# Kernel tuning notes

Measured on AMD Instinct MI355X. Metric: run time of the kernel, lower is better.

The kernel has to match this reference:

```python
import jax, jax.numpy as jnp
import numpy as np
from jax import lax

D_MODEL = 64
D_STATE = 16
D_CONV = 3
EXPAND = 2
D_INNER = EXPAND * D_MODEL  # 128
DT_RANK = (D_MODEL + 15) // 16  # 4
B, H, W = 2, 64, 64


def setup_inputs() -> dict:
    key = jax.random.key(0)
    ks = jax.random.split(key, 8)
    def n(k, shape, s=0.02):
        return jax.random.normal(k, shape, dtype=jnp.float32) * s
    return {
        "x": jax.random.normal(ks[0], (B, D_MODEL, H, W), dtype=jnp.float32),
        "ln_w": jnp.ones((D_MODEL,), jnp.float32),
        "ln_b": jnp.zeros((D_MODEL,), jnp.float32),
        "W_in": n(ks[1], (4, 2 * D_INNER, D_MODEL)),          # in_proj per direction
        "conv_w": n(ks[2], (4, D_INNER, 1, D_CONV), 0.1),     # depthwise causal conv
        "conv_b": jnp.zeros((4, D_INNER), jnp.float32),
        "W_xproj": n(ks[3], (4, DT_RANK + 2 * D_STATE, D_INNER)),
        "W_dt": n(ks[4], (4, D_INNER, DT_RANK), 0.1),
        "b_dt": n(ks[5], (4, D_INNER), 0.1),
        "A_log": jnp.log(jnp.broadcast_to(jnp.arange(1, D_STATE + 1, dtype=jnp.float32), (4, D_INNER, D_STATE))),
        "D_param": jnp.ones((4, D_INNER), jnp.float32),
        "W_out": n(ks[6], (4, D_MODEL, D_INNER)),
    }


def _mamba(x, W_in, conv_w, conv_b, W_xproj, W_dt, b_dt, A_log, Dp, W_out):
    # x: (B, L, D) -> (B, L, D). Standard Mamba forward with selective scan.
    xz = x @ W_in.T                              # (B, L, 2*d_inner)
    xp, z = jnp.split(xz, 2, axis=-1)
    xc = jnp.swapaxes(xp, 1, 2)                  # (B, d_inner, L)
    xc = lax.conv_general_dilated(xc, conv_w, (1,), [(D_CONV - 1, 0)], feature_group_count=D_INNER)
    xc = xc + conv_b[None, :, None]
    xp = jax.nn.silu(jnp.swapaxes(xc, 1, 2))     # (B, L, d_inner)
    dbl = xp @ W_xproj.T                         # (B, L, dt_rank + 2*d_state)
    dt = dbl[..., :DT_RANK]
    Bc = dbl[..., DT_RANK:DT_RANK + D_STATE]
    Cc = dbl[..., DT_RANK + D_STATE:]
    dt = jax.nn.softplus(dt @ W_dt.T + b_dt)     # (B, L, d_inner)
    A = -jnp.exp(A_log)                          # (d_inner, d_state)
    dA = jnp.exp(dt[..., None] * A)              # (B, L, d_inner, d_state)
    dBu = (dt * xp)[..., None] * Bc[:, :, None, :]

    def comb(c1, c2):
        a1, b1 = c1
        a2, b2 = c2
        return a1 * a2, a2 * b1 + b2

    _, h = lax.associative_scan(comb, (dA, dBu), axis=1)  # parallel linear recurrence
    y = jnp.einsum('blds,bls->bld', h, Cc) + xp * Dp
    y = y * jax.nn.silu(z)
    return y @ W_out.T


def reference(x, ln_w, ln_b, W_in, conv_w, conv_b, W_xproj, W_dt, b_dt, A_log, D_param, W_out):
    Bq, C, Hh, Ww = x.shape
    xn = jnp.transpose(x, (0, 2, 3, 1))          # (B, H, W, C)
    mu = xn.mean(-1, keepdims=True)
    var = xn.var(-1, keepdims=True)
    xn = (xn - mu) * lax.rsqrt(var + 1e-5) * ln_w + ln_b
    x_f = xn.reshape(Bq, Hh * Ww, C)                              # row-major scan
    x_tf = jnp.transpose(xn, (0, 2, 1, 3)).reshape(Bq, Ww * Hh, C)  # column-major scan
    xs = jnp.stack([x_f, x_f[:, ::-1], x_tf, x_tf[:, ::-1]])      # (4, B, L, C)
    ys = jax.vmap(_mamba)(xs, W_in, conv_w, conv_b, W_xproj, W_dt, b_dt, A_log, D_param, W_out)
    y = ys[0].reshape(Bq, Hh, Ww, C) + ys[1][:, ::-1].reshape(Bq, Hh, Ww, C)
    yt = ys[2].reshape(Bq, Ww, Hh, C) + ys[3][:, ::-1].reshape(Bq, Ww, Hh, C)
    y = y + jnp.transpose(yt, (0, 2, 1, 3))
    return jnp.transpose(y, (0, 3, 1, 2))        # back to (B, C, H, W)
```

## Files before the change

### kernel.cpp

```cpp
#include <hip/hip_runtime.h>
#include <math.h>


#define PP  8
#define LL  4096
#define DD  128
#define SS  16
#define CH  32
#define NCH 128

__device__ __forceinline__ float sigmoidf_(float x){ return 1.0f/(1.0f+__expf(-x)); }

__global__ __launch_bounds__(256) void k_ln(const float* __restrict__ x,
    const float* __restrict__ lw, const float* __restrict__ lb, float* __restrict__ xn) {
  int tid = threadIdx.x;
  int lane = tid & 63;
  int pos = blockIdx.x*4 + (tid>>6);
  int b = pos >> 12, hw = pos & 4095;
  float v = x[((long)(b*64 + lane))*4096 + hw];
  float s = v;
  for (int m = 32; m; m >>= 1) s += __shfl_xor(s, m);
  float mu = s * (1.0f/64.0f);
  float dv = (v-mu)*(v-mu);
  for (int m = 32; m; m >>= 1) dv += __shfl_xor(dv, m);
  float rs = rsqrtf(dv*(1.0f/64.0f) + 1e-5f);
  xn[(long)pos*64 + lane] = (v-mu)*rs*lw[lane] + lb[lane];
}

__global__ __launch_bounds__(256) void k_xseq(const float* __restrict__ xn, float* __restrict__ xseq) {
  int gid = blockIdx.x*256 + threadIdx.x;
  int c = gid & 63;
  int t = (gid >> 6) & 4095;
  int p = gid >> 18;
  int b = p & 1, dir = p >> 1;
  int l;
  if (dir == 0) l = t;
  else if (dir == 1) l = 4095 - t;
  else {
    int tt = (dir == 2) ? t : 4095 - t;
    l = ((tt & 63) << 6) | (tt >> 6);
  }
  xseq[gid] = xn[((long)(b*4096 + l))*64 + c];
}

__global__ __launch_bounds__(256) void k_gemm(const float* __restrict__ A, const float* __restrict__ Bw,
    float* __restrict__ C, int M, int N, int K, long aStr, long bStr, long cStr) {
  __shared__ float Ast[64][68];
  __shared__ float Bst[64][68];
  int pair = blockIdx.z;
  const float* Ap = A + (long)pair*aStr;
  const float* Bp = Bw + (long)(pair>>1)*bStr;
  float* Cp = C + (long)pair*cStr;
  int tid = threadIdx.x;
  int tx = tid & 15, ty = tid >> 4;
  int m0 = blockIdx.x*64, n0 = blockIdx.y*64;
  int kk4 = tid & 15, rr = tid >> 4;
  float acc[4][4] = {};
  for (int ko = 0; ko < K; ko += 64) {
    for (int pass = 0; pass < 4; ++pass) {
      int r = pass*16 + rr;
      float4 av = *(const float4*)(Ap + (long)(m0+r)*K + ko + kk4*4);
      Ast[kk4*4+0][r]=av.x; Ast[kk4*4+1][r]=av.y; Ast[kk4*4+2][r]=av.z; Ast[kk4*4+3][r]=av.w;
      int j = n0 + r;
      float4 bv = make_float4(0.f,0.f,0.f,0.f);
      if (j < N) bv = *(const float4*)(Bp + (long)j*K + ko + kk4*4);
      Bst[kk4*4+0][r]=bv.x; Bst[kk4*4+1][r]=bv.y; Bst[kk4*4+2][r]=bv.z; Bst[kk4*4+3][r]=bv.w;
    }
    __syncthreads();
    #pragma unroll 8
    for (int kk = 0; kk < 64; ++kk) {
      float4 a = *(const float4*)(&Ast[kk][ty*4]);
      float4 b = *(const float4*)(&Bst[kk][tx*4]);
      acc[0][0] += a.x*b.x; acc[0][1] += a.x*b.y; acc[0][2] += a.x*b.z; acc[0][3] += a.x*b.w;
      acc[1][0] += a.y*b.x; acc[1][1] += a.y*b.y; acc[1][2] += a.y*b.z; acc[1][3] += a.y*b.w;
      acc[2][0] += a.z*b.x; acc[2][1] += a.z*b.y; acc[2][2] += a.z*b.z; acc[2][3] += a.z*b.w;
      acc[3][0] += a.w*b.x; acc[3][1] += a.w*b.y; acc[3][2] += a.w*b.z; acc[3][3] += a.w*b.w;
    }
    __syncthreads();
  }
  for (int i = 0; i < 4; ++i)
    for (int j = 0; j < 4; ++j) {
      int m = m0 + ty*4 + i, n = n0 + tx*4 + j;
      if (n < N) Cp[(long)m*N + n] = acc[i][j];
    }
}

__global__ __launch_bounds__(256) void k_conv(const float* __restrict__ xz, const float* __restrict__ cw,
    const float* __restrict__ cb, float* __restrict__ u) {
  int gid = blockIdx.x*256 + threadIdx.x;
  int d = gid & 127;
  int t = (gid >> 7) & 4095;
  int p = gid >> 19;
  int dir = p >> 1;
  const float* base = xz + ((long)p*4096)*256 + d;
  float x2 = base[(long)t*256];
  float x1 = (t >= 1) ? base[(long)(t-1)*256] : 0.f;
  float x0 = (t >= 2) ? base[(long)(t-2)*256] : 0.f;
  const float* w = cw + (dir*128 + d)*3;
  float a = x0*w[0] + x1*w[1] + x2*w[2] + cb[dir*128 + d];
  u[gid] = a * sigmoidf_(a);
}

__global__ __launch_bounds__(256) void k_dt(const float* __restrict__ dbl, const float* __restrict__ wdt,
    const float* __restrict__ bdt, float* __restrict__ dt) {
  int gid = blockIdx.x*256 + threadIdx.x;
  int d = gid & 127;
  int t = (gid >> 7) & 4095;
  int p = gid >> 19;
  int dir = p >> 1;
  const float* r = dbl + ((long)p*4096 + t)*36;
  float4 w = *(const float4*)(wdt + ((dir*128 + d) << 2));
  float lin = r[0]*w.x + r[1]*w.y + r[2]*w.z + r[3]*w.w + bdt[dir*128 + d];
  float sp = (lin > 20.f) ? lin : log1pf(__expf(lin));
  dt[gid] = sp;
}

__global__ __launch_bounds__(128) void k_scan1(const float* __restrict__ dt, const float* __restrict__ u,
    const float* __restrict__ dbl, const float* __restrict__ alog,
    float* __restrict__ pend, float* __restrict__ dAc) {
  int ch = blockIdx.x, p = blockIdx.y, dir = p >> 1;
  int d = threadIdx.x;
  __shared__ float Bsm[CH*16];
  long rowbase = (long)p*LL + ch*CH;
  #pragma unroll
  for (int k = 0; k < 4; ++k) {
    int idx = d + k*128;
    int t = idx >> 4, j = idx & 15;
    Bsm[idx] = dbl[(rowbase + t)*36 + 4 + j];
  }
  float A[16], ps[16];
  const float* ab = alog + ((dir*DD + d) << 4);
  #pragma unroll
  for (int s = 0; s < 16; ++s) { A[s] = -__expf(ab[s]); ps[s] = 0.f; }
  float sd = 0.f;
  __syncthreads();
  for (int t = 0; t < CH; ++t) {
    long row = rowbase + t;
    float dtv = dt[row*DD + d];
    float uv  = u [row*DD + d];
    float dtu = dtv*uv;
    sd += dtv;
    const float* Bs = &Bsm[t*16];
    #pragma unroll
    for (int s = 0; s < 16; ++s) {
      float dA = __expf(dtv*A[s]);
      ps[s] = fmaf(dA, ps[s], dtu*Bs[s]);
    }
  }
  long base = ((long)(p*NCH + ch)*DD + d)*16;
  #pragma unroll
  for (int s = 0; s < 16; ++s) {
    pend[base+s] = ps[s];
    dAc [base+s] = __expf(A[s]*sd);
  }
}

__global__ __launch_bounds__(256) void k_scan2(const float* __restrict__ pend,
    const float* __restrict__ dAc, float* __restrict__ carry) {
  int g = blockIdx.x*256 + threadIdx.x;
  long hi = ((long)(g >> 11)) << 18;
  int lo = g & 2047;
  float c = 0.f;
  for (int chk = 0; chk < NCH; ++chk) {
    long idx = hi + ((long)chk << 11) + lo;
    carry[idx] = c;
    c = fmaf(dAc[idx], c, pend[idx]);
  }
}

__global__ __launch_bounds__(128) void k_scan3(const float* __restrict__ dt, const float* __restrict__ u,
    const float* __restrict__ dbl, const float* __restrict__ xz, const float* __restrict__ alog,
    const float* __restrict__ Dp, const float* __restrict__ carry, float* __restrict__ y) {
  int ch = blockIdx.x, p = blockIdx.y, dir = p >> 1;
  int d = threadIdx.x;
  __shared__ float Bsm[CH*16];
  __shared__ float Csm[CH*16];
  long rowbase = (long)p*LL + ch*CH;
  #pragma unroll
  for (int k = 0; k < 8; ++k) {
    int idx = d + k*128;
    int half = idx >> 9;
    int e = idx & 511;
    int t = e >> 4, j = e & 15;
    float v = dbl[(rowbase + t)*36 + (half ? 20 : 4) + j];
    if (half) Csm[e] = v; else Bsm[e] = v;
  }
  float A[16], h[16];
  const float* ab = alog + ((dir*DD + d) << 4);
  long cbase = ((long)(p*NCH + ch)*DD + d)*16;
  #pragma unroll
  for (int s = 0; s < 16; ++s) {
    A[s] = -__expf(ab[s]);
    h[s] = carry[cbase + s];
  }
  float Dv = Dp[dir*DD + d];
  __syncthreads();
  for (int t = 0; t < CH; ++t) {
    long row = rowbase + t;
    float dtv = dt[row*DD + d];
    float uv  = u [row*DD + d];
    float zv  = xz[row*256 + 128 + d];
    float dtu = dtv*uv;
    const float* Bs = &Bsm[t*16];
    const float* Cs = &Csm[t*16];
    float acc = 0.f;
    #pragma unroll
    for (int s = 0; s < 16; ++s) {
      float dA = __expf(dtv*A[s]);
      h[s] = fmaf(dA, h[s], dtu*Bs[s]);
      acc = fmaf(h[s], Cs[s], acc);
    }
    float yv = acc + uv*Dv;
    yv *= zv * sigmoidf_(zv);
    y[row*DD + d] = yv;
  }
}

__global__ __launch_bounds__(256) void k_comb(const float* __restrict__ yg, float* __restrict__ out) {
  int o = blockIdx.x*256 + threadIdx.x;
  int w = o & 63, h = (o>>6)&63, c = (o>>12)&63, b = o>>18;
  int t0 = (h<<6)|w, t2 = (w<<6)|h;
  float v = yg[((long)(b*4096) + t0)*64 + c]
          + yg[((long)((2+b)*4096) + (4095 - t0))*64 + c]
          + yg[((long)((4+b)*4096) + t2)*64 + c]
          + yg[((long)((6+b)*4096) + (4095 - t2))*64 + c];
  out[o] = v;
}

extern "C" void kernel_launch(void* const* d_in, const int* in_sizes, int n_in,
                              void* d_out, int out_size, void* d_ws, size_t ws_size,
                              hipStream_t stream) {
  const float* x      = (const float*)d_in[0];
  const float* ln_w   = (const float*)d_in[1];
  const float* ln_b   = (const float*)d_in[2];
  const float* W_in   = (const float*)d_in[3];
  const float* conv_w = (const float*)d_in[4];
  const float* conv_b = (const float*)d_in[5];
  const float* W_xp   = (const float*)d_in[6];
  const float* W_dt   = (const float*)d_in[7];
  const float* b_dt   = (const float*)d_in[8];
  const float* A_log  = (const float*)d_in[9];
  const float* D_par  = (const float*)d_in[10];
  const float* W_out  = (const float*)d_in[11];

  float* ws    = (float*)d_ws;
  float* xn    = ws;
  float* xseq  = xn    + 524288;
  float* xz    = xseq  + 2097152;
  float* u     = xz    + 8388608;
  float* dblb  = u     + 4194304;
  float* dtb   = dblb  + 1179648;
  float* ybuf  = dtb   + 4194304;
  float* yg    = ybuf  + 4194304;
  float* pend  = ybuf;
  float* dAc   = ybuf  + 2097152;
  float* carry = xseq;

  k_ln  <<<2048, 256, 0, stream>>>(x, ln_w, ln_b, xn);
  k_xseq<<<8192, 256, 0, stream>>>(xn, xseq);
  k_gemm<<<dim3(64,4,8), 256, 0, stream>>>(xseq, W_in, xz, 4096, 256, 64,
                                           4096L*64, 256L*64, 4096L*256);
  k_conv<<<16384, 256, 0, stream>>>(xz, conv_w, conv_b, u);
  k_gemm<<<dim3(64,1,8), 256, 0, stream>>>(u, W_xp, dblb, 4096, 36, 128,
                                           4096L*128, 36L*128, 4096L*36);
  k_dt  <<<16384, 256, 0, stream>>>(dblb, W_dt, b_dt, dtb);
  k_scan1<<<dim3(NCH,PP), 128, 0, stream>>>(dtb, u, dblb, A_log, pend, dAc);
  k_scan2<<<64, 256, 0, stream>>>(pend, dAc, carry);
  k_scan3<<<dim3(NCH,PP), 128, 0, stream>>>(dtb, u, dblb, xz, A_log, D_par, carry, ybuf);
  k_gemm<<<dim3(64,1,8), 256, 0, stream>>>(ybuf, W_out, yg, 4096, 64, 128,
                                           4096L*128, 64L*128, 4096L*64);
  k_comb<<<2048, 256, 0, stream>>>(yg, (float*)d_out);
}
```

Before: 245.9 us.

## Fuse direction gather into in_proj GEMM and dt projection into scan kernels

Removes the k_xseq permutation kernel by having a specialized in_proj GEMM gather rows from the normalized input through a direction map. Removes the k_dt kernel and its 4M-float buffer by recomputing softplus(dt projection) inside both scan passes from the dbl rows. Reshapes scan2 into more, smaller blocks for more parallelism, and rewrites the final combine to transpose through shared memory so output stores are coalesced. The cost is duplicated dt math in scan1 and scan3 and a separate workspace for carry/pend.

```diff
diff --git a/kernel.cpp b/kernel.cpp
--- a/kernel.cpp
+++ b/kernel.cpp
@@ -5,11 +5,17 @@
 #define PP  8
 #define LL  4096
 #define DD  128
-#define SS  16
 #define CH  32
 #define NCH 128
 
 __device__ __forceinline__ float sigmoidf_(float x){ return 1.0f/(1.0f+__expf(-x)); }
+
+__device__ __forceinline__ int dirmap(int dir, int t) {
+  if (dir == 0) return t;
+  if (dir == 1) return 4095 - t;
+  int tt = (dir == 2) ? t : 4095 - t;
+  return ((tt & 63) << 6) | (tt >> 6);
+}
 
 __global__ __launch_bounds__(256) void k_ln(const float* __restrict__ x,
     const float* __restrict__ lw, const float* __restrict__ lb, float* __restrict__ xn) {
@@ -27,20 +33,41 @@
   xn[(long)pos*64 + lane] = (v-mu)*rs*lw[lane] + lb[lane];
 }
 
-__global__ __launch_bounds__(256) void k_xseq(const float* __restrict__ xn, float* __restrict__ xseq) {
-  int gid = blockIdx.x*256 + threadIdx.x;
-  int c = gid & 63;
-  int t = (gid >> 6) & 4095;
-  int p = gid >> 18;
-  int b = p & 1, dir = p >> 1;
-  int l;
-  if (dir == 0) l = t;
-  else if (dir == 1) l = 4095 - t;
-  else {
-    int tt = (dir == 2) ? t : 4095 - t;
-    l = ((tt & 63) << 6) | (tt >> 6);
-  }
-  xseq[gid] = xn[((long)(b*4096 + l))*64 + c];
+__global__ __launch_bounds__(256) void k_gemm1(const float* __restrict__ xn,
+    const float* __restrict__ Win, float* __restrict__ xz) {
+  __shared__ float Ast[64][68];
+  __shared__ float Bst[64][68];
+  int p = blockIdx.z, dir = p >> 1, b = p & 1;
+  int tid = threadIdx.x;
+  int tx = tid & 15, ty = tid >> 4;
+  int m0 = blockIdx.x*64, n0 = blockIdx.y*64;
+  int kk4 = tid & 15, rr = tid >> 4;
+  #pragma unroll
+  for (int pass = 0; pass < 4; ++pass) {
+    int r = pass*16 + rr;
+    int l = dirmap(dir, m0 + r);
+    float4 av = *(const float4*)(xn + ((long)(b*4096 + l))*64 + kk4*4);
+    Ast[kk4*4+0][r]=av.x; Ast[kk4*4+1][r]=av.y; Ast[kk4*4+2][r]=av.z; Ast[kk4*4+3][r]=av.w;
+    float4 bv = *(const float4*)(Win + ((long)(dir*256 + n0 + r))*64 + kk4*4);
+    Bst[kk4*4+0][r]=bv.x; Bst[kk4*4+1][r]=bv.y; Bst[kk4*4+2][r]=bv.z; Bst[kk4*4+3][r]=bv.w;
+  }
+  __syncthreads();
+  float acc[4][4] = {};
+  #pragma unroll 8
+  for (int kk = 0; kk < 64; ++kk) {
+    float4 a = *(const float4*)(&Ast[kk][ty*4]);
+    float4 bq = *(const float4*)(&Bst[kk][tx*4]);
+    acc[0][0] += a.x*bq.x; acc[0][1] += a.x*bq.y; acc[0][2] += a.x*bq.z; acc[0][3] += a.x*bq.w;
+    acc[1][0] += a.y*bq.x; acc[1][1] += a.y*bq.y; acc[1][2] += a.y*bq.z; acc[1][3] += a.y*bq.w;
+    acc[2][0] += a.z*bq.x; acc[2][1] += a.z*bq.y; acc[2][2] += a.z*bq.z; acc[2][3] += a.z*bq.w;
+    acc[3][0] += a.w*bq.x; acc[3][1] += a.w*bq.y; acc[3][2] += a.w*bq.z; acc[3][3] += a.w*bq.w;
+  }
+  float* Cp = xz + (long)p*4096*256;
+  #pragma unroll
+  for (int i = 0; i < 4; ++i)
+    #pragma unroll
+    for (int j = 0; j < 4; ++j)
+      Cp[(long)(m0 + ty*4 + i)*256 + n0 + tx*4 + j] = acc[i][j];
 }
 
 __global__ __launch_bounds__(256) void k_gemm(const float* __restrict__ A, const float* __restrict__ Bw,
@@ -101,23 +128,9 @@
   u[gid] = a * sigmoidf_(a);
 }
 
-__global__ __launch_bounds__(256) void k_dt(const float* __restrict__ dbl, const float* __restrict__ wdt,
-    const float* __restrict__ bdt, float* __restrict__ dt) {
-  int gid = blockIdx.x*256 + threadIdx.x;
-  int d = gid & 127;
-  int t = (gid >> 7) & 4095;
-  int p = gid >> 19;
-  int dir = p >> 1;
-  const float* r = dbl + ((long)p*4096 + t)*36;
-  float4 w = *(const float4*)(wdt + ((dir*128 + d) << 2));
-  float lin = r[0]*w.x + r[1]*w.y + r[2]*w.z + r[3]*w.w + bdt[dir*128 + d];
-  float sp = (lin > 20.f) ? lin : log1pf(__expf(lin));
-  dt[gid] = sp;
-}
-
-__global__ __launch_bounds__(128) void k_scan1(const float* __restrict__ dt, const float* __restrict__ u,
-    const float* __restrict__ dbl, const float* __restrict__ alog,
-    float* __restrict__ pend, float* __restrict__ dAc) {
+__global__ __launch_bounds__(128) void k_scan1(const float* __restrict__ u,
+    const float* __restrict__ dbl, const float* __restrict__ wdt, const float* __restrict__ bdt,
+    const float* __restrict__ alog, float* __restrict__ pend, float* __restrict__ dAc) {
   int ch = blockIdx.x, p = blockIdx.y, dir = p >> 1;
   int d = threadIdx.x;
   __shared__ float Bsm[CH*16];
@@ -125,9 +138,10 @@
   #pragma unroll
   for (int k = 0; k < 4; ++k) {
     int idx = d + k*128;
-    int t = idx >> 4, j = idx & 15;
-    Bsm[idx] = dbl[(rowbase + t)*36 + 4 + j];
-  }
+    Bsm[idx] = dbl[(rowbase + (idx >> 4))*36 + 4 + (idx & 15)];
+  }
+  float4 wv = *(const float4*)(wdt + ((dir*DD + d) << 2));
+  float bv = bdt[dir*DD + d];
   float A[16], ps[16];
   const float* ab = alog + ((dir*DD + d) << 4);
   #pragma unroll
@@ -136,8 +150,10 @@
   __syncthreads();
   for (int t = 0; t < CH; ++t) {
     long row = rowbase + t;
-    float dtv = dt[row*DD + d];
-    float uv  = u [row*DD + d];
+    float4 r4 = *(const float4*)(dbl + row*36);
+    float lin = r4.x*wv.x + r4.y*wv.y + r4.z*wv.z + r4.w*wv.w + bv;
+    float dtv = (lin > 20.f) ? lin : log1pf(__expf(lin));
+    float uv  = u[row*DD + d];
     float dtu = dtv*uv;
     sd += dtv;
     const float* Bs = &Bsm[t*16];
@@ -155,9 +171,9 @@
   }
 }
 
-__global__ __launch_bounds__(256) void k_scan2(const float* __restrict__ pend,
+__global__ __launch_bounds__(64) void k_scan2(const float* __restrict__ pend,
     const float* __restrict__ dAc, float* __restrict__ carry) {
-  int g = blockIdx.x*256 + threadIdx.x;
+  int g = blockIdx.x*64 + threadIdx.x;
   long hi = ((long)(g >> 11)) << 18;
   int lo = g & 2047;
   float c = 0.f;
@@ -168,8 +184,9 @@
   }
 }
 
-__global__ __launch_bounds__(128) void k_scan3(const float* __restrict__ dt, const float* __restrict__ u,
-    const float* __restrict__ dbl, const float* __restrict__ xz, const float* __restrict__ alog,
+__global__ __launch_bounds__(128) void k_scan3(const float* __restrict__ u,
+    const float* __restrict__ dbl, const float* __restrict__ wdt, const float* __restrict__ bdt,
+    const float* __restrict__ xz, const float* __restrict__ alog,
     const float* __restrict__ Dp, const float* __restrict__ carry, float* __restrict__ y) {
   int ch = blockIdx.x, p = blockIdx.y, dir = p >> 1;
   int d = threadIdx.x;
@@ -181,10 +198,11 @@
     int idx = d + k*128;
     int half = idx >> 9;
     int e = idx & 511;
-    int t = e >> 4, j = e & 15;
-    float v = dbl[(rowbase + t)*36 + (half ? 20 : 4) + j];
+    float v = dbl[(rowbase + (e >> 4))*36 + (half ? 20 : 4) + (e & 15)];
     if (half) Csm[e] = v; else Bsm[e] = v;
   }
+  float4 wv = *(const float4*)(wdt + ((dir*DD + d) << 2));
+  float bvb = bdt[dir*DD + d];
   float A[16], h[16];
   const float* ab = alog + ((dir*DD + d) << 4);
   long cbase = ((long)(p*NCH + ch)*DD + d)*16;
@@ -197,7 +215,9 @@
   __syncthreads();
   for (int t = 0; t < CH; ++t) {
     long row = rowbase + t;
-    float dtv = dt[row*DD + d];
+    float4 r4 = *(const float4*)(dbl + row*36);
+    float lin = r4.x*wv.x + r4.y*wv.y + r4.z*wv.z + r4.w*wv.w + bvb;
+    float dtv = (lin > 20.f) ? lin : log1pf(__expf(lin));
     float uv  = u [row*DD + d];
     float zv  = xz[row*256 + 128 + d];
     float dtu = dtv*uv;
@@ -217,14 +237,29 @@
 }
 
 __global__ __launch_bounds__(256) void k_comb(const float* __restrict__ yg, float* __restrict__ out) {
-  int o = blockIdx.x*256 + threadIdx.x;
-  int w = o & 63, h = (o>>6)&63, c = (o>>12)&63, b = o>>18;
-  int t0 = (h<<6)|w, t2 = (w<<6)|h;
-  float v = yg[((long)(b*4096) + t0)*64 + c]
-          + yg[((long)((2+b)*4096) + (4095 - t0))*64 + c]
-          + yg[((long)((4+b)*4096) + t2)*64 + c]
-          + yg[((long)((6+b)*4096) + (4095 - t2))*64 + c];
-  out[o] = v;
+  __shared__ float ysm[64][65];
+  int bh = blockIdx.x;
+  int b = bh >> 6, h = bh & 63;
+  int tid = threadIdx.x;
+  int c = tid & 63, q = tid >> 6;
+  #pragma unroll
+  for (int i = 0; i < 16; ++i) {
+    int w = q*16 + i;
+    int t0 = (h << 6) | w;
+    int t2 = (w << 6) | h;
+    float v = yg[((long)(b*4096) + t0)*64 + c]
+            + yg[((long)((2+b)*4096) + (4095 - t0))*64 + c]
+            + yg[((long)((4+b)*4096) + t2)*64 + c]
+            + yg[((long)((6+b)*4096) + (4095 - t2))*64 + c];
+    ysm[w][c] = v;
+  }
+  __syncthreads();
+  int w2 = tid & 63;
+  #pragma unroll
+  for (int i = 0; i < 16; ++i) {
+    int cc = q*16 + i;
+    out[((long)(b*64 + cc))*4096 + (h << 6) + w2] = ysm[w2][cc];
+  }
 }
 
 extern "C" void kernel_launch(void* const* d_in, const int* in_sizes, int n_in,
@@ -245,29 +280,24 @@
 
   float* ws    = (float*)d_ws;
   float* xn    = ws;
-  float* xseq  = xn    + 524288;
-  float* xz    = xseq  + 2097152;
+  float* xz    = xn    + 524288;
   float* u     = xz    + 8388608;
   float* dblb  = u     + 4194304;
-  float* dtb   = dblb  + 1179648;
-  float* ybuf  = dtb   + 4194304;
+  float* pend  = dblb  + 1179648;
+  float* dAc   = pend  + 2097152;
+  float* carry = dAc   + 2097152;
+  float* ybuf  = carry + 2097152;
   float* yg    = ybuf  + 4194304;
-  float* pend  = ybuf;
-  float* dAc   = ybuf  + 2097152;
-  float* carry = xseq;
-
-  k_ln  <<<2048, 256, 0, stream>>>(x, ln_w, ln_b, xn);
-  k_xseq<<<8192, 256, 0, stream>>>(xn, xseq);
-  k_gemm<<<dim3(64,4,8), 256, 0, stream>>>(xseq, W_in, xz, 4096, 256, 64,
-                                           4096L*64, 256L*64, 4096L*256);
-  k_conv<<<16384, 256, 0, stream>>>(xz, conv_w, conv_b, u);
-  k_gemm<<<dim3(64,1,8), 256, 0, stream>>>(u, W_xp, dblb, 4096, 36, 128,
-                                           4096L*128, 36L*128, 4096L*36);
-  k_dt  <<<16384, 256, 0, stream>>>(dblb, W_dt, b_dt, dtb);
-  k_scan1<<<dim3(NCH,PP), 128, 0, stream>>>(dtb, u, dblb, A_log, pend, dAc);
-  k_scan2<<<64, 256, 0, stream>>>(pend, dAc, carry);
-  k_scan3<<<dim3(NCH,PP), 128, 0, stream>>>(dtb, u, dblb, xz, A_log, D_par, carry, ybuf);
-  k_gemm<<<dim3(64,1,8), 256, 0, stream>>>(ybuf, W_out, yg, 4096, 64, 128,
-                                           4096L*128, 64L*128, 4096L*64);
-  k_comb<<<2048, 256, 0, stream>>>(yg, (float*)d_out);
-}
+
+  k_ln   <<<2048, 256, 0, stream>>>(x, ln_w, ln_b, xn);
+  k_gemm1<<<dim3(64,4,8), 256, 0, stream>>>(xn, W_in, xz);
+  k_conv <<<16384, 256, 0, stream>>>(xz, conv_w, conv_b, u);
+  k_gemm <<<dim3(64,1,8), 256, 0, stream>>>(u, W_xp, dblb, 4096, 36, 128,
+                                            4096L*128, 36L*128, 4096L*36);
+  k_scan1<<<dim3(NCH,PP), 128, 0, stream>>>(u, dblb, W_dt, b_dt, A_log, pend, dAc);
+  k_scan2<<<256, 64, 0, stream>>>(pend, dAc, carry);
+  k_scan3<<<dim3(NCH,PP), 128, 0, stream>>>(u, dblb, W_dt, b_dt, xz, A_log, D_par, carry, ybuf);
+  k_gemm <<<dim3(64,1,8), 256, 0, stream>>>(ybuf, W_out, yg, 4096, 64, 128,
+                                            4096L*128, 64L*128, 4096L*64);
+  k_comb <<<128, 256, 0, stream>>>(yg, (float*)d_out);
+}
```

Result: slower. 257.4 us (+4.7%).
